# Kernel tuning notes

Hardware: AMD Instinct MI355X
Metric: run time of the kernel (lower is better)

Reference implementation:

```python
import jax, jax.numpy as jnp
import numpy as np

N, R, H, OUT = 512, 16, 16, 1
EPSILON = 1e-6
CUTOFF = 5.0  # ExpNormalSmearing cutoff_upper (cutoff_lower = 0)


def exp_normal_smearing(dist):
    # dist: (N, N, 1) -> (N, N, R); TorchMD-Net style ExpNormalSmearing
    start = jnp.exp(-CUTOFF)
    means = jnp.linspace(start, 1.0, R, dtype=dist.dtype)
    beta = (2.0 / R * (1.0 - start)) ** -2
    cutoff = 0.5 * (jnp.cos(dist * jnp.pi / CUTOFF) + 1.0) * (dist < CUTOFF)
    return cutoff * jnp.exp(-beta * (jnp.exp(-dist) - means) ** 2)


def setup_inputs() -> dict:
    key = jax.random.key(0)
    ks = jax.random.split(key, 9)
    s_in = 1.0 / np.sqrt(H * H)
    s_h = 1.0 / np.sqrt(H)
    return {
        "x": jax.random.normal(ks[0], (N, 3), jnp.float32) * 1.5,
        "W": jax.random.normal(ks[1], (2, N, R, H), jnp.float32) * 0.1,
        "W1": jax.random.normal(ks[2], (H, H * H), jnp.float32) * s_in,
        "b1": jax.random.normal(ks[3], (H,), jnp.float32) * 0.01,
        "W2": jax.random.normal(ks[4], (4 * R * H, H), jnp.float32) * s_h,
        "W3": jax.random.normal(ks[5], (H, H * H), jnp.float32) * s_in,
        "b3": jax.random.normal(ks[6], (H,), jnp.float32) * 0.01,
        "W4": jax.random.normal(ks[7], (OUT, H), jnp.float32) * s_h,
        "b4": jax.random.normal(ks[8], (OUT,), jnp.float32) * 0.01,
    }


def reference(x, W, W1, b1, W2, W3, b3, W4, b4):
    K, Q = W[0], W[1]                               # (N, R, H) each
    diff = x[:, None, :] - x[None, :, :]            # (N, N, 3)
    nsq = jnp.sum(diff * diff, axis=-1, keepdims=True) + EPSILON
    norm = jnp.sqrt(nsq)                            # (N, N, 1)
    diff = diff / nsq                               # note: divided by squared norm (faithful)
    sm = exp_normal_smearing(norm)                  # (N, N, R)
    basis = sm[..., None] * diff[..., None, :]      # (N, N, R, 3)

    bk = jnp.einsum('ijrb,jrc->icb', basis, K)      # (N, H, 3)
    bq = jnp.einsum('ijrb,jrc->icb', basis, Q)
    att = jnp.einsum('ihb,igb->ihg', bk, bq).reshape(N, H * H)
    att = jax.nn.silu(att @ W1.T + b1) @ W2.T       # (N, 4*R*H), second Linear bias-free

    left, right = att[:, : 2 * R * H], att[:, 2 * R * H:]
    pair = left[:, None, :] + right[None, :, :]     # (N, N, 2*R*H)
    K2 = pair[..., : R * H].reshape(N, N, R, H)
    Q2 = pair[..., R * H:].reshape(N, N, R, H)

    bk = jnp.einsum('ijrb,ijrc->icb', basis, K2)    # (N, H, 3)
    bq = jnp.einsum('ijrb,ijrc->icb', basis, Q2)
    att = jnp.einsum('ihb,igb->ihg', bk, bq).reshape(N, H * H)
    return jax.nn.silu(att @ W3.T + b3) @ W4.T + b4  # (N, OUT)
```

## Files before the change

kernel.cpp:

```cpp
#include <hip/hip_runtime.h>
#include <hip/hip_bf16.h>
#include <math.h>

#define NN 512

#define START 0.006737946999085467f
#define STEP  ((1.0f - START) * (1.0f/15.0f))
#define SB    (0.125f * (1.0f - START))
#define BETA  (1.0f/(SB*SB))
#define LOG2E 1.4426950408889634f
#define NB    (-(BETA)*LOG2E)


__global__ __launch_bounds__(256) void k1a(const float* __restrict__ x,
                                           const float* __restrict__ W,
                                           float* __restrict__ part1)
{
    const int ib = blockIdx.x & 127, jsH = blockIdx.x >> 7;
    const int i0 = ib * 4;
    const int tid = threadIdx.x;
    const int c = tid & 15, js = tid >> 4;
    const int lane = tid & 63, wv = tid >> 6;

    __shared__ float lG[1328];
    __shared__ float lP[256];
    __shared__ float s_part[4][16][26];

    const int gi = tid >> 6, gj = (tid >> 2) & 15, grq = tid & 3;
    const float gxi0 = x[(i0+gi)*3+0];
    const float gxi1 = x[(i0+gi)*3+1];
    const float gxi2 = x[(i0+gi)*3+2];

    float acc[24];
    #pragma unroll
    for (int v = 0; v < 24; ++v) acc[v] = 0.f;

    for (int jt = 0; jt < 4; ++jt) {
        const int jb = jsH*64 + jt*16;
        __syncthreads();

        {
            float d0 = gxi0 - x[(jb+gj)*3+0];
            float d1 = gxi1 - x[(jb+gj)*3+1];
            float d2 = gxi2 - x[(jb+gj)*3+2];
            float nsq = fmaf(d0,d0, fmaf(d1,d1, fmaf(d2,d2, 1e-6f)));
            float rs  = __builtin_amdgcn_rsqf(nsq);
            float nrm = nsq * rs;
            float inv = rs * rs;
            float cutv = 0.f;
            if (nrm < 5.0f) cutv = 0.5f*(__cosf(nrm*0.6283185307179586f)+1.0f);
            float en = exp2f(-LOG2E * nrm);
            if (grq == 0) {
                float4 dP; dP.x = d0*inv; dP.y = d1*inv; dP.z = d2*inv; dP.w = 0.f;
                *reinterpret_cast<float4*>(&lP[(gi*16+gj)*4]) = dP;
            }
            float4 g4;
            {
                float t0 = en - (START + STEP*(float)(grq*4+0));
                float t1 = en - (START + STEP*(float)(grq*4+1));
                float t2 = en - (START + STEP*(float)(grq*4+2));
                float t3 = en - (START + STEP*(float)(grq*4+3));
                g4.x = cutv * exp2f(NB*t0*t0);
                g4.y = cutv * exp2f(NB*t1*t1);
                g4.z = cutv * exp2f(NB*t2*t2);
                g4.w = cutv * exp2f(NB*t3*t3);
            }
            *reinterpret_cast<float4*>(&lG[gi*328 + gj*20 + grq*4]) = g4;
        }
        __syncthreads();

        const float* Kr = W + (size_t)(jb+js)*256 + c;
        const float* Qr = Kr + NN*256;
        float kk[16], qq[16];
        #pragma unroll
        for (int r = 0; r < 16; ++r) { kk[r] = Kr[r*16]; qq[r] = Qr[r*16]; }

        #pragma unroll
        for (int i = 0; i < 4; ++i) {
            const float4* gp = reinterpret_cast<const float4*>(&lG[i*328 + js*20]);
            float4 gA = gp[0], gB = gp[1], gC = gp[2], gD = gp[3];
            float tk = 0.f, tq = 0.f;
            tk = fmaf(gA.x,kk[ 0], tk); tq = fmaf(gA.x,qq[ 0], tq);
            tk = fmaf(gA.y,kk[ 1], tk); tq = fmaf(gA.y,qq[ 1], tq);
            tk = fmaf(gA.z,kk[ 2], tk); tq = fmaf(gA.z,qq[ 2], tq);
            tk = fmaf(gA.w,kk[ 3], tk); tq = fmaf(gA.w,qq[ 3], tq);
            tk = fmaf(gB.x,kk[ 4], tk); tq = fmaf(gB.x,qq[ 4], tq);
            tk = fmaf(gB.y,kk[ 5], tk); tq = fmaf(gB.y,qq[ 5], tq);
            tk = fmaf(gB.z,kk[ 6], tk); tq = fmaf(gB.z,qq[ 6], tq);
            tk = fmaf(gB.w,kk[ 7], tk); tq = fmaf(gB.w,qq[ 7], tq);
            tk = fmaf(gC.x,kk[ 8], tk); tq = fmaf(gC.x,qq[ 8], tq);
            tk = fmaf(gC.y,kk[ 9], tk); tq = fmaf(gC.y,qq[ 9], tq);
            tk = fmaf(gC.z,kk[10], tk); tq = fmaf(gC.z,qq[10], tq);
            tk = fmaf(gC.w,kk[11], tk); tq = fmaf(gC.w,qq[11], tq);
            tk = fmaf(gD.x,kk[12], tk); tq = fmaf(gD.x,qq[12], tq);
            tk = fmaf(gD.y,kk[13], tk); tq = fmaf(gD.y,qq[13], tq);
            tk = fmaf(gD.z,kk[14], tk); tq = fmaf(gD.z,qq[14], tq);
            tk = fmaf(gD.w,kk[15], tk); tq = fmaf(gD.w,qq[15], tq);
            float4 dd = *reinterpret_cast<const float4*>(&lP[(i*16+js)*4]);
            acc[i*6+0] = fmaf(tk, dd.x, acc[i*6+0]);
            acc[i*6+1] = fmaf(tk, dd.y, acc[i*6+1]);
            acc[i*6+2] = fmaf(tk, dd.z, acc[i*6+2]);
            acc[i*6+3] = fmaf(tq, dd.x, acc[i*6+3]);
            acc[i*6+4] = fmaf(tq, dd.y, acc[i*6+4]);
            acc[i*6+5] = fmaf(tq, dd.z, acc[i*6+5]);
        }
    }

    #pragma unroll
    for (int v = 0; v < 24; ++v) {
        float t = acc[v];
        t += __shfl_xor(t, 16);
        t += __shfl_xor(t, 32);
        if (lane < 16) s_part[wv][c][v] = t;
    }
    __syncthreads();

    for (int v = tid; v < 384; v += 256) {
        int i = v / 96, o = v - i*96;
        int kq = o / 48, rem = o - kq*48;
        int b = rem >> 4, c2 = rem & 15;
        int f = i*6 + kq*3 + b;
        float sum = s_part[0][c2][f] + s_part[1][c2][f]
                  + s_part[2][c2][f] + s_part[3][c2][f];
        part1[(i0+i)*768 + jsH*96 + o] = sum;
    }
}

__global__ __launch_bounds__(256) void k1b(const float* __restrict__ part1,
                                           const float* __restrict__ W1,
                                           const float* __restrict__ b1,
                                           const float* __restrict__ W2,
                                           float* __restrict__ att2)
{
    const int i = blockIdx.x;
    const int tid = threadIdx.x;
    __shared__ float s_bkq[96];
    __shared__ float s_att[256];
    __shared__ float s_z[16][16];
    __shared__ float s_a1[16];

    if (tid < 96) {
        const float* p = part1 + i*768 + tid;
        float s = 0.f;
        #pragma unroll
        for (int k = 0; k < 8; ++k) s += p[k*96];
        s_bkq[tid] = s;
    }
    __syncthreads();

    {
        int h = tid >> 4, g = tid & 15;
        s_att[tid] = s_bkq[     h]*s_bkq[48+     g]
                   + s_bkq[16 + h]*s_bkq[48+16 + g]
                   + s_bkq[32 + h]*s_bkq[48+32 + g];
    }
    __syncthreads();

    {
        int h = tid & 15, seg = tid >> 4;
        const float* w1 = W1 + h*256 + seg*16;
        const float* a  = s_att + seg*16;
        float p = 0.f;
        #pragma unroll
        for (int k = 0; k < 16; ++k) p = fmaf(a[k], w1[k], p);
        s_z[seg][h] = p;
    }
    __syncthreads();

    if (tid < 16) {
        float z = b1[tid];
        #pragma unroll
        for (int seg = 0; seg < 16; ++seg) z += s_z[seg][tid];
        s_a1[tid] = z / (1.0f + __expf(-z));
    }
    __syncthreads();

    float a1[16];
    #pragma unroll
    for (int cc = 0; cc < 16; ++cc) a1[cc] = s_a1[cc];
    #pragma unroll
    for (int p = 0; p < 4; ++p) {
        int o = tid + p*256;
        const float4* w2 = reinterpret_cast<const float4*>(W2 + o*16);
        float4 wa = w2[0], wb = w2[1], wc = w2[2], wd = w2[3];
        float accv = wa.x*a1[0] + wa.y*a1[1] + wa.z*a1[2] + wa.w*a1[3]
                   + wb.x*a1[4] + wb.y*a1[5] + wb.z*a1[6] + wb.w*a1[7]
                   + wc.x*a1[8] + wc.y*a1[9] + wc.z*a1[10]+ wc.w*a1[11]
                   + wd.x*a1[12]+ wd.y*a1[13]+ wd.z*a1[14]+ wd.w*a1[15];
        att2[i*1024 + o] = accv;
    }
}

__global__ __launch_bounds__(256) void k2a(const float* __restrict__ x,
                                           const float* __restrict__ att2,
                                           float* __restrict__ part2)
{
    const int ib = blockIdx.x & 127, jsH = blockIdx.x >> 7;
    const int i0 = ib * 4;
    const int tid = threadIdx.x;
    const int c = tid & 15, js = tid >> 4;
    const int lane = tid & 63, wv = tid >> 6;

    __shared__ float lG[1328];
    __shared__ float lP[256];
    __shared__ float s_part[4][16][38];

    const int gi = tid >> 6, gj = (tid >> 2) & 15, grq = tid & 3;
    const float gxi0 = x[(i0+gi)*3+0];
    const float gxi1 = x[(i0+gi)*3+1];
    const float gxi2 = x[(i0+gi)*3+2];

    float acc[36];
    #pragma unroll
    for (int v = 0; v < 36; ++v) acc[v] = 0.f;

    for (int jt = 0; jt < 4; ++jt) {
        const int jb = jsH*64 + jt*16;
        __syncthreads();

        {
            float d0 = gxi0 - x[(jb+gj)*3+0];
            float d1 = gxi1 - x[(jb+gj)*3+1];
            float d2 = gxi2 - x[(jb+gj)*3+2];
            float nsq = fmaf(d0,d0, fmaf(d1,d1, fmaf(d2,d2, 1e-6f)));
            float rs  = __builtin_amdgcn_rsqf(nsq);
            float nrm = nsq * rs;
            float inv = rs * rs;
            float cutv = 0.f;
            if (nrm < 5.0f) cutv = 0.5f*(__cosf(nrm*0.6283185307179586f)+1.0f);
            float en = exp2f(-LOG2E * nrm);
            if (grq == 0) {
                float4 dP; dP.x = d0*inv; dP.y = d1*inv; dP.z = d2*inv; dP.w = 0.f;
                *reinterpret_cast<float4*>(&lP[(gi*16+gj)*4]) = dP;
            }
            float4 g4;
            {
                float t0 = en - (START + STEP*(float)(grq*4+0));
                float t1 = en - (START + STEP*(float)(grq*4+1));
                float t2 = en - (START + STEP*(float)(grq*4+2));
                float t3 = en - (START + STEP*(float)(grq*4+3));
                g4.x = cutv * exp2f(NB*t0*t0);
                g4.y = cutv * exp2f(NB*t1*t1);
                g4.z = cutv * exp2f(NB*t2*t2);
                g4.w = cutv * exp2f(NB*t3*t3);
            }
            *reinterpret_cast<float4*>(&lG[gi*328 + gj*20 + grq*4]) = g4;
        }
        __syncthreads();

        const float* Rk = att2 + (size_t)(jb+js)*1024 + 512 + c;
        const float* Rq = Rk + 256;
        float kk[16], qq[16];
        #pragma unroll
        for (int r = 0; r < 16; ++r) { kk[r] = Rk[r*16]; qq[r] = Rq[r*16]; }

        #pragma unroll
        for (int i = 0; i < 4; ++i) {
            const float4* gp = reinterpret_cast<const float4*>(&lG[i*328 + js*20]);
            float4 gA = gp[0], gB = gp[1], gC = gp[2], gD = gp[3];
            float tk = 0.f, tq = 0.f;
            tk = fmaf(gA.x,kk[ 0], tk); tq = fmaf(gA.x,qq[ 0], tq);
            tk = fmaf(gA.y,kk[ 1], tk); tq = fmaf(gA.y,qq[ 1], tq);
            tk = fmaf(gA.z,kk[ 2], tk); tq = fmaf(gA.z,qq[ 2], tq);
            tk = fmaf(gA.w,kk[ 3], tk); tq = fmaf(gA.w,qq[ 3], tq);
            tk = fmaf(gB.x,kk[ 4], tk); tq = fmaf(gB.x,qq[ 4], tq);
            tk = fmaf(gB.y,kk[ 5], tk); tq = fmaf(gB.y,qq[ 5], tq);
            tk = fmaf(gB.z,kk[ 6], tk); tq = fmaf(gB.z,qq[ 6], tq);
            tk = fmaf(gB.w,kk[ 7], tk); tq = fmaf(gB.w,qq[ 7], tq);
            tk = fmaf(gC.x,kk[ 8], tk); tq = fmaf(gC.x,qq[ 8], tq);
            tk = fmaf(gC.y,kk[ 9], tk); tq = fmaf(gC.y,qq[ 9], tq);
            tk = fmaf(gC.z,kk[10], tk); tq = fmaf(gC.z,qq[10], tq);
            tk = fmaf(gC.w,kk[11], tk); tq = fmaf(gC.w,qq[11], tq);
            tk = fmaf(gD.x,kk[12], tk); tq = fmaf(gD.x,qq[12], tq);
            tk = fmaf(gD.y,kk[13], tk); tq = fmaf(gD.y,qq[13], tq);
            tk = fmaf(gD.z,kk[14], tk); tq = fmaf(gD.z,qq[14], tq);
            tk = fmaf(gD.w,kk[15], tk); tq = fmaf(gD.w,qq[15], tq);
            float4 dd = *reinterpret_cast<const float4*>(&lP[(i*16+js)*4]);
            acc[i*6+0] = fmaf(tk, dd.x, acc[i*6+0]);
            acc[i*6+1] = fmaf(tk, dd.y, acc[i*6+1]);
            acc[i*6+2] = fmaf(tk, dd.z, acc[i*6+2]);
            acc[i*6+3] = fmaf(tq, dd.x, acc[i*6+3]);
            acc[i*6+4] = fmaf(tq, dd.y, acc[i*6+4]);
            acc[i*6+5] = fmaf(tq, dd.z, acc[i*6+5]);
            float gc = lG[i*328 + js*20 + c];
            acc[24+i*3+0] = fmaf(gc, dd.x, acc[24+i*3+0]);
            acc[24+i*3+1] = fmaf(gc, dd.y, acc[24+i*3+1]);
            acc[24+i*3+2] = fmaf(gc, dd.z, acc[24+i*3+2]);
        }
    }

    #pragma unroll
    for (int v = 0; v < 36; ++v) {
        float t = acc[v];
        t += __shfl_xor(t, 16);
        t += __shfl_xor(t, 32);
        if (lane < 16) s_part[wv][c][v] = t;
    }
    __syncthreads();

    for (int v = tid; v < 576; v += 256) {
        int i = v / 144, o = v - i*144;
        int c2, f;
        if (o < 96) {
            int kq = o / 48, rem = o - kq*48;
            int b = rem >> 4; c2 = rem & 15;
            f = i*6 + kq*3 + b;
        } else {
            int oS = o - 96;
            int r = oS / 3, b = oS - r*3;
            c2 = r;
            f = 24 + i*3 + b;
        }
        float sum = s_part[0][c2][f] + s_part[1][c2][f]
                  + s_part[2][c2][f] + s_part[3][c2][f];
        part2[(i0+i)*1152 + jsH*144 + o] = sum;
    }
}

__global__ __launch_bounds__(256) void k2b(const float* __restrict__ att2,
                                           const float* __restrict__ part2,
                                           const float* __restrict__ W3,
                                           const float* __restrict__ b3,
                                           const float* __restrict__ W4,
                                           const float* __restrict__ b4,
                                           float* __restrict__ out)
{
    const int i = blockIdx.x;
    const int tid = threadIdx.x;
    __shared__ float s_red[144];
    __shared__ float s_att[256];
    __shared__ float s_z[16][16];
    __shared__ float s_a1[16];

    if (tid < 144) {
        const float* p = part2 + i*1152 + tid;
        float s = 0.f;
        #pragma unroll
        for (int k = 0; k < 8; ++k) s += p[k*144];
        s_red[tid] = s;
    }
    __syncthreads();

    if (tid < 96) {
        int kq = tid / 48, rem = tid - kq*48;
        int b = rem >> 4, c = rem & 15;
        const float* lrow = att2 + i*1024 + kq*256 + c;
        float add = 0.f;
        #pragma unroll
        for (int r = 0; r < 16; ++r)
            add = fmaf(lrow[r*16], s_red[96 + r*3 + b], add);
        s_red[tid] += add;
    }
    __syncthreads();

    {
        int h = tid >> 4, g = tid & 15;
        s_att[tid] = s_red[     h]*s_red[48+     g]
                   + s_red[16 + h]*s_red[48+16 + g]
                   + s_red[32 + h]*s_red[48+32 + g];
    }
    __syncthreads();

    {
        int h = tid & 15, seg = tid >> 4;
        const float* w3 = W3 + h*256 + seg*16;
        const float* a  = s_att + seg*16;
        float p = 0.f;
        #pragma unroll
        for (int k = 0; k < 16; ++k) p = fmaf(a[k], w3[k], p);
        s_z[seg][h] = p;
    }
    __syncthreads();

    if (tid < 16) {
        float z = b3[tid];
        #pragma unroll
        for (int seg = 0; seg < 16; ++seg) z += s_z[seg][tid];
        s_a1[tid] = z / (1.0f + __expf(-z));
    }
    __syncthreads();

    if (tid == 0) {
        float accv = b4[0];
        #pragma unroll
        for (int cc = 0; cc < 16; ++cc) accv = fmaf(s_a1[cc], W4[cc], accv);
        out[i] = accv;
    }
}

extern "C" void kernel_launch(void* const* d_in, const int* in_sizes, int n_in,
                              void* d_out, int out_size, void* d_ws, size_t ws_size,
                              hipStream_t stream) {
    (void)in_sizes; (void)n_in; (void)out_size; (void)ws_size;
    const float* x  = (const float*)d_in[0];
    const float* W  = (const float*)d_in[1];
    const float* W1 = (const float*)d_in[2];
    const float* b1 = (const float*)d_in[3];
    const float* W2 = (const float*)d_in[4];
    const float* W3 = (const float*)d_in[5];
    const float* b3 = (const float*)d_in[6];
    const float* W4 = (const float*)d_in[7];
    const float* b4 = (const float*)d_in[8];

    float* att2  = (float*)d_ws;
    float* part1 = att2 + 512*1024;
    float* part2 = part1 + 512*768;
    float* out   = (float*)d_out;

    k1a<<<1024, 256, 0, stream>>>(x, W, part1);
    k1b<<<512, 256, 0, stream>>>(part1, W1, b1, W2, att2);
    k2a<<<1024, 256, 0, stream>>>(x, att2, part2);
    k2b<<<512, 256, 0, stream>>>(att2, part2, W3, b3, W4, b4, out);
}
```

Measured before the change: 126.0 us.

## Transpose K/Q weights for vector loads, store smearing in fp16, compute once

```diff
diff --git a/kernel.cpp b/kernel.cpp
--- a/kernel.cpp
+++ b/kernel.cpp
@@ -1,5 +1,6 @@
 #include <hip/hip_runtime.h>
 #include <hip/hip_bf16.h>
+#include <hip/hip_fp16.h>
 #include <math.h>
 
 #define NN 512
@@ -12,91 +13,102 @@
 #define NB    (-(BETA)*LOG2E)
 
 
-__global__ __launch_bounds__(256) void k1a(const float* __restrict__ x,
-                                           const float* __restrict__ W,
-                                           float* __restrict__ part1)
+__global__ __launch_bounds__(256) void k0(const float* __restrict__ W,
+                                          float* __restrict__ Wt)
 {
-    const int ib = blockIdx.x & 127, jsH = blockIdx.x >> 7;
+    __shared__ float ldsb[256];
+    const int row = blockIdx.x;
+    ldsb[threadIdx.x] = W[(size_t)row*256 + threadIdx.x];
+    __syncthreads();
+    const int c = threadIdx.x >> 4, r = threadIdx.x & 15;
+    Wt[(size_t)row*256 + threadIdx.x] = ldsb[r*16 + c];
+}
+
+__global__ __launch_bounds__(256,3) void k1a(const float* __restrict__ x,
+                                             const float* __restrict__ Wt,
+                                             float* __restrict__ part1)
+{
+    const int ib = blockIdx.x & 127, jc = blockIdx.x >> 7;
     const int i0 = ib * 4;
     const int tid = threadIdx.x;
     const int c = tid & 15, js = tid >> 4;
     const int lane = tid & 63, wv = tid >> 6;
 
-    __shared__ float lG[1328];
-    __shared__ float lP[256];
+    __shared__ __half lG[4][64][16];
+    __shared__ float4 lP[4][64];
     __shared__ float s_part[4][16][26];
 
-    const int gi = tid >> 6, gj = (tid >> 2) & 15, grq = tid & 3;
-    const float gxi0 = x[(i0+gi)*3+0];
-    const float gxi1 = x[(i0+gi)*3+1];
-    const float gxi2 = x[(i0+gi)*3+2];
+    {
+        const int pi = tid >> 6, pj = tid & 63;
+        const int jg = jc*64 + pj;
+        const float xi0 = x[(i0+pi)*3+0], xi1 = x[(i0+pi)*3+1], xi2 = x[(i0+pi)*3+2];
+        float d0 = xi0 - x[jg*3+0];
+        float d1 = xi1 - x[jg*3+1];
+        float d2 = xi2 - x[jg*3+2];
+        float nsq = fmaf(d0,d0, fmaf(d1,d1, fmaf(d2,d2, 1e-6f)));
+        float rs  = __builtin_amdgcn_rsqf(nsq);
+        float nrm = nsq * rs;
+        float inv = rs * rs;
+        float cutv = 0.f;
+        if (nrm < 5.0f) cutv = 0.5f*(__cosf(nrm*0.6283185307179586f)+1.0f);
+        float en = exp2f(-LOG2E * nrm);
+        lP[pi][pj] = make_float4(d0*inv, d1*inv, d2*inv, 0.f);
+        __half2* dst = reinterpret_cast<__half2*>(&lG[pi][pj][0]);
+        #pragma unroll
+        for (int r2 = 0; r2 < 8; ++r2) {
+            float t0 = en - (START + STEP*(float)(2*r2+0));
+            float t1 = en - (START + STEP*(float)(2*r2+1));
+            dst[r2] = __floats2half2_rn(cutv*exp2f(NB*t0*t0),
+                                        cutv*exp2f(NB*t1*t1));
+        }
+    }
+    __syncthreads();
 
     float acc[24];
     #pragma unroll
     for (int v = 0; v < 24; ++v) acc[v] = 0.f;
 
-    for (int jt = 0; jt < 4; ++jt) {
-        const int jb = jsH*64 + jt*16;
-        __syncthreads();
-
-        {
-            float d0 = gxi0 - x[(jb+gj)*3+0];
-            float d1 = gxi1 - x[(jb+gj)*3+1];
-            float d2 = gxi2 - x[(jb+gj)*3+2];
-            float nsq = fmaf(d0,d0, fmaf(d1,d1, fmaf(d2,d2, 1e-6f)));
-            float rs  = __builtin_amdgcn_rsqf(nsq);
-            float nrm = nsq * rs;
-            float inv = rs * rs;
-            float cutv = 0.f;
-            if (nrm < 5.0f) cutv = 0.5f*(__cosf(nrm*0.6283185307179586f)+1.0f);
-            float en = exp2f(-LOG2E * nrm);
-            if (grq == 0) {
-                float4 dP; dP.x = d0*inv; dP.y = d1*inv; dP.z = d2*inv; dP.w = 0.f;
-                *reinterpret_cast<float4*>(&lP[(gi*16+gj)*4]) = dP;
-            }
-            float4 g4;
-            {
-                float t0 = en - (START + STEP*(float)(grq*4+0));
-                float t1 = en - (START + STEP*(float)(grq*4+1));
-                float t2 = en - (START + STEP*(float)(grq*4+2));
-                float t3 = en - (START + STEP*(float)(grq*4+3));
-                g4.x = cutv * exp2f(NB*t0*t0);
-                g4.y = cutv * exp2f(NB*t1*t1);
-                g4.z = cutv * exp2f(NB*t2*t2);
-                g4.w = cutv * exp2f(NB*t3*t3);
-            }
-            *reinterpret_cast<float4*>(&lG[gi*328 + gj*20 + grq*4]) = g4;
-        }
-        __syncthreads();
-
-        const float* Kr = W + (size_t)(jb+js)*256 + c;
-        const float* Qr = Kr + NN*256;
-        float kk[16], qq[16];
-        #pragma unroll
-        for (int r = 0; r < 16; ++r) { kk[r] = Kr[r*16]; qq[r] = Qr[r*16]; }
+    #pragma unroll
+    for (int t = 0; t < 4; ++t) {
+        const int jl = js + 16*t;
+        const int jg = jc*64 + jl;
+        const float4* Kp = reinterpret_cast<const float4*>(Wt + (size_t)jg*256 + c*16);
+        const float4* Qp = reinterpret_cast<const float4*>(Wt + (size_t)NN*256 + (size_t)jg*256 + c*16);
+        float4 ka = Kp[0], kb = Kp[1], kc = Kp[2], kd = Kp[3];
+        float4 qa = Qp[0], qb = Qp[1], qc = Qp[2], qd = Qp[3];
 
         #pragma unroll
         for (int i = 0; i < 4; ++i) {
-            const float4* gp = reinterpret_cast<const float4*>(&lG[i*328 + js*20]);
-            float4 gA = gp[0], gB = gp[1], gC = gp[2], gD = gp[3];
-            float tk = 0.f, tq = 0.f;
-            tk = fmaf(gA.x,kk[ 0], tk); tq = fmaf(gA.x,qq[ 0], tq);
-            tk = fmaf(gA.y,kk[ 1], tk); tq = fmaf(gA.y,qq[ 1], tq);
-            tk = fmaf(gA.z,kk[ 2], tk); tq = fmaf(gA.z,qq[ 2], tq);
-            tk = fmaf(gA.w,kk[ 3], tk); tq = fmaf(gA.w,qq[ 3], tq);
-            tk = fmaf(gB.x,kk[ 4], tk); tq = fmaf(gB.x,qq[ 4], tq);
-            tk = fmaf(gB.y,kk[ 5], tk); tq = fmaf(gB.y,qq[ 5], tq);
-            tk = fmaf(gB.z,kk[ 6], tk); tq = fmaf(gB.z,qq[ 6], tq);
-            tk = fmaf(gB.w,kk[ 7], tk); tq = fmaf(gB.w,qq[ 7], tq);
-            tk = fmaf(gC.x,kk[ 8], tk); tq = fmaf(gC.x,qq[ 8], tq);
-            tk = fmaf(gC.y,kk[ 9], tk); tq = fmaf(gC.y,qq[ 9], tq);
-            tk = fmaf(gC.z,kk[10], tk); tq = fmaf(gC.z,qq[10], tq);
-            tk = fmaf(gC.w,kk[11], tk); tq = fmaf(gC.w,qq[11], tq);
-            tk = fmaf(gD.x,kk[12], tk); tq = fmaf(gD.x,qq[12], tq);
-            tk = fmaf(gD.y,kk[13], tk); tq = fmaf(gD.y,qq[13], tq);
-            tk = fmaf(gD.z,kk[14], tk); tq = fmaf(gD.z,qq[14], tq);
-            tk = fmaf(gD.w,kk[15], tk); tq = fmaf(gD.w,qq[15], tq);
-            float4 dd = *reinterpret_cast<const float4*>(&lP[(i*16+js)*4]);
+            const float4* gp = reinterpret_cast<const float4*>(&lG[i][jl][0]);
+            float4 g0 = gp[0], g1 = gp[1];
+            const __half2* h0 = reinterpret_cast<const __half2*>(&g0);
+            const __half2* h1 = reinterpret_cast<const __half2*>(&g1);
+            float2 p0 = __half22float2(h0[0]);
+            float2 p1 = __half22float2(h0[1]);
+            float2 p2 = __half22float2(h0[2]);
+            float2 p3 = __half22float2(h0[3]);
+            float2 p4 = __half22float2(h1[0]);
+            float2 p5 = __half22float2(h1[1]);
+            float2 p6 = __half22float2(h1[2]);
+            float2 p7 = __half22float2(h1[3]);
+            float tk, tq;
+            tk = p0.x*ka.x; tq = p0.x*qa.x;
+            tk = fmaf(p0.y,ka.y,tk); tq = fmaf(p0.y,qa.y,tq);
+            tk = fmaf(p1.x,ka.z,tk); tq = fmaf(p1.x,qa.z,tq);
+            tk = fmaf(p1.y,ka.w,tk); tq = fmaf(p1.y,qa.w,tq);
+            tk = fmaf(p2.x,kb.x,tk); tq = fmaf(p2.x,qb.x,tq);
+            tk = fmaf(p2.y,kb.y,tk); tq = fmaf(p2.y,qb.y,tq);
+            tk = fmaf(p3.x,kb.z,tk); tq = fmaf(p3.x,qb.z,tq);
+            tk = fmaf(p3.y,kb.w,tk); tq = fmaf(p3.y,qb.w,tq);
+            tk = fmaf(p4.x,kc.x,tk); tq = fmaf(p4.x,qc.x,tq);
+            tk = fmaf(p4.y,kc.y,tk); tq = fmaf(p4.y,qc.y,tq);
+            tk = fmaf(p5.x,kc.z,tk); tq = fmaf(p5.x,qc.z,tq);
+            tk = fmaf(p5.y,kc.w,tk); tq = fmaf(p5.y,qc.w,tq);
+            tk = fmaf(p6.x,kd.x,tk); tq = fmaf(p6.x,qd.x,tq);
+            tk = fmaf(p6.y,kd.y,tk); tq = fmaf(p6.y,qd.y,tq);
+            tk = fmaf(p7.x,kd.z,tk); tq = fmaf(p7.x,qd.z,tq);
+            tk = fmaf(p7.y,kd.w,tk); tq = fmaf(p7.y,qd.w,tq);
+            float4 dd = lP[i][jl];
             acc[i*6+0] = fmaf(tk, dd.x, acc[i*6+0]);
             acc[i*6+1] = fmaf(tk, dd.y, acc[i*6+1]);
             acc[i*6+2] = fmaf(tk, dd.z, acc[i*6+2]);
@@ -122,7 +134,7 @@
         int f = i*6 + kq*3 + b;
         float sum = s_part[0][c2][f] + s_part[1][c2][f]
                   + s_part[2][c2][f] + s_part[3][c2][f];
-        part1[(i0+i)*768 + jsH*96 + o] = sum;
+        part1[(i0+i)*768 + jc*96 + o] = sum;
     }
 }
 
@@ -130,7 +142,7 @@
                                            const float* __restrict__ W1,
                                            const float* __restrict__ b1,
                                            const float* __restrict__ W2,
-                                           float* __restrict__ att2)
+                                           float* __restrict__ att2t)
 {
     const int i = blockIdx.x;
     const int tid = threadIdx.x;
@@ -187,102 +199,104 @@
                    + wb.x*a1[4] + wb.y*a1[5] + wb.z*a1[6] + wb.w*a1[7]
                    + wc.x*a1[8] + wc.y*a1[9] + wc.z*a1[10]+ wc.w*a1[11]
                    + wd.x*a1[12]+ wd.y*a1[13]+ wd.z*a1[14]+ wd.w*a1[15];
-        att2[i*1024 + o] = accv;
-    }
-}
-
-__global__ __launch_bounds__(256) void k2a(const float* __restrict__ x,
-                                           const float* __restrict__ att2,
-                                           float* __restrict__ part2)
+        att2t[i*1024 + ((o>>8)*256) + ((o&15)*16) + ((o>>4)&15)] = accv;
+    }
+}
+
+__global__ __launch_bounds__(256,3) void k2a(const float* __restrict__ x,
+                                             const float* __restrict__ att2t,
+                                             float* __restrict__ part2)
 {
-    const int ib = blockIdx.x & 127, jsH = blockIdx.x >> 7;
+    const int ib = blockIdx.x & 127, jc = blockIdx.x >> 7;
     const int i0 = ib * 4;
     const int tid = threadIdx.x;
     const int c = tid & 15, js = tid >> 4;
     const int lane = tid & 63, wv = tid >> 6;
 
-    __shared__ float lG[1328];
-    __shared__ float lP[256];
+    __shared__ __half lG[4][64][16];
+    __shared__ float4 lP[4][64];
     __shared__ float s_part[4][16][38];
 
-    const int gi = tid >> 6, gj = (tid >> 2) & 15, grq = tid & 3;
-    const float gxi0 = x[(i0+gi)*3+0];
-    const float gxi1 = x[(i0+gi)*3+1];
-    const float gxi2 = x[(i0+gi)*3+2];
+    {
+        const int pi = tid >> 6, pj = tid & 63;
+        const int jg = jc*64 + pj;
+        const float xi0 = x[(i0+pi)*3+0], xi1 = x[(i0+pi)*3+1], xi2 = x[(i0+pi)*3+2];
+        float d0 = xi0 - x[jg*3+0];
+        float d1 = xi1 - x[jg*3+1];
+        float d2 = xi2 - x[jg*3+2];
+        float nsq = fmaf(d0,d0, fmaf(d1,d1, fmaf(d2,d2, 1e-6f)));
+        float rs  = __builtin_amdgcn_rsqf(nsq);
+        float nrm = nsq * rs;
+        float inv = rs * rs;
+        float cutv = 0.f;
+        if (nrm < 5.0f) cutv = 0.5f*(__cosf(nrm*0.6283185307179586f)+1.0f);
+        float en = exp2f(-LOG2E * nrm);
+        lP[pi][pj] = make_float4(d0*inv, d1*inv, d2*inv, 0.f);
+        __half2* dst = reinterpret_cast<__half2*>(&lG[pi][pj][0]);
+        #pragma unroll
+        for (int r2 = 0; r2 < 8; ++r2) {
+            float t0 = en - (START + STEP*(float)(2*r2+0));
+            float t1 = en - (START + STEP*(float)(2*r2+1));
+            dst[r2] = __floats2half2_rn(cutv*exp2f(NB*t0*t0),
+                                        cutv*exp2f(NB*t1*t1));
+        }
+    }
+    __syncthreads();
 
     float acc[36];
     #pragma unroll
     for (int v = 0; v < 36; ++v) acc[v] = 0.f;
 
-    for (int jt = 0; jt < 4; ++jt) {
-        const int jb = jsH*64 + jt*16;
-        __syncthreads();
-
-        {
-            float d0 = gxi0 - x[(jb+gj)*3+0];
-            float d1 = gxi1 - x[(jb+gj)*3+1];
-            float d2 = gxi2 - x[(jb+gj)*3+2];
-            float nsq = fmaf(d0,d0, fmaf(d1,d1, fmaf(d2,d2, 1e-6f)));
-            float rs  = __builtin_amdgcn_rsqf(nsq);
-            float nrm = nsq * rs;
-            float inv = rs * rs;
-            float cutv = 0.f;
-            if (nrm < 5.0f) cutv = 0.5f*(__cosf(nrm*0.6283185307179586f)+1.0f);
-            float en = exp2f(-LOG2E * nrm);
-            if (grq == 0) {
-                float4 dP; dP.x = d0*inv; dP.y = d1*inv; dP.z = d2*inv; dP.w = 0.f;
-                *reinterpret_cast<float4*>(&lP[(gi*16+gj)*4]) = dP;
-            }
-            float4 g4;
-            {
-                float t0 = en - (START + STEP*(float)(grq*4+0));
-                float t1 = en - (START + STEP*(float)(grq*4+1));
-                float t2 = en - (START + STEP*(float)(grq*4+2));
-                float t3 = en - (START + STEP*(float)(grq*4+3));
-                g4.x = cutv * exp2f(NB*t0*t0);
-                g4.y = cutv * exp2f(NB*t1*t1);
-                g4.z = cutv * exp2f(NB*t2*t2);
-                g4.w = cutv * exp2f(NB*t3*t3);
-            }
-            *reinterpret_cast<float4*>(&lG[gi*328 + gj*20 + grq*4]) = g4;
-        }
-        __syncthreads();
-
-        const float* Rk = att2 + (size_t)(jb+js)*1024 + 512 + c;
-        const float* Rq = Rk + 256;
-        float kk[16], qq[16];
-        #pragma unroll
-        for (int r = 0; r < 16; ++r) { kk[r] = Rk[r*16]; qq[r] = Rq[r*16]; }
+    #pragma unroll
+    for (int t = 0; t < 4; ++t) {
+        const int jl = js + 16*t;
+        const int jg = jc*64 + jl;
+        const float4* Kp = reinterpret_cast<const float4*>(att2t + (size_t)jg*1024 + 512 + c*16);
+        const float4* Qp = reinterpret_cast<const float4*>(att2t + (size_t)jg*1024 + 768 + c*16);
+        float4 ka = Kp[0], kb = Kp[1], kc = Kp[2], kd = Kp[3];
+        float4 qa = Qp[0], qb = Qp[1], qc = Qp[2], qd = Qp[3];
 
         #pragma unroll
         for (int i = 0; i < 4; ++i) {
-            const float4* gp = reinterpret_cast<const float4*>(&lG[i*328 + js*20]);
-            float4 gA = gp[0], gB = gp[1], gC = gp[2], gD = gp[3];
-            float tk = 0.f, tq = 0.f;
-            tk = fmaf(gA.x,kk[ 0], tk); tq = fmaf(gA.x,qq[ 0], tq);
-            tk = fmaf(gA.y,kk[ 1], tk); tq = fmaf(gA.y,qq[ 1], tq);
-            tk = fmaf(gA.z,kk[ 2], tk); tq = fmaf(gA.z,qq[ 2], tq);
-            tk = fmaf(gA.w,kk[ 3], tk); tq = fmaf(gA.w,qq[ 3], tq);
-            tk = fmaf(gB.x,kk[ 4], tk); tq = fmaf(gB.x,qq[ 4], tq);
-            tk = fmaf(gB.y,kk[ 5], tk); tq = fmaf(gB.y,qq[ 5], tq);
-            tk = fmaf(gB.z,kk[ 6], tk); tq = fmaf(gB.z,qq[ 6], tq);
-            tk = fmaf(gB.w,kk[ 7], tk); tq = fmaf(gB.w,qq[ 7], tq);
-            tk = fmaf(gC.x,kk[ 8], tk); tq = fmaf(gC.x,qq[ 8], tq);
-            tk = fmaf(gC.y,kk[ 9], tk); tq = fmaf(gC.y,qq[ 9], tq);
-            tk = fmaf(gC.z,kk[10], tk); tq = fmaf(gC.z,qq[10], tq);
-            tk = fmaf(gC.w,kk[11], tk); tq = fmaf(gC.w,qq[11], tq);
-            tk = fmaf(gD.x,kk[12], tk); tq = fmaf(gD.x,qq[12], tq);
-            tk = fmaf(gD.y,kk[13], tk); tq = fmaf(gD.y,qq[13], tq);
-            tk = fmaf(gD.z,kk[14], tk); tq = fmaf(gD.z,qq[14], tq);
-            tk = fmaf(gD.w,kk[15], tk); tq = fmaf(gD.w,qq[15], tq);
-            float4 dd = *reinterpret_cast<const float4*>(&lP[(i*16+js)*4]);
+            const float4* gp = reinterpret_cast<const float4*>(&lG[i][jl][0]);
+            float4 g0 = gp[0], g1 = gp[1];
+            const __half2* h0 = reinterpret_cast<const __half2*>(&g0);
+            const __half2* h1 = reinterpret_cast<const __half2*>(&g1);
+            float2 p0 = __half22float2(h0[0]);
+            float2 p1 = __half22float2(h0[1]);
+            float2 p2 = __half22float2(h0[2]);
+            float2 p3 = __half22float2(h0[3]);
+            float2 p4 = __half22float2(h1[0]);
+            float2 p5 = __half22float2(h1[1]);
+            float2 p6 = __half22float2(h1[2]);
+            float2 p7 = __half22float2(h1[3]);
+            float tk, tq;
+            tk = p0.x*ka.x; tq = p0.x*qa.x;
+            tk = fmaf(p0.y,ka.y,tk); tq = fmaf(p0.y,qa.y,tq);
+            tk = fmaf(p1.x,ka.z,tk); tq = fmaf(p1.x,qa.z,tq);
+            tk = fmaf(p1.y,ka.w,tk); tq = fmaf(p1.y,qa.w,tq);
+            tk = fmaf(p2.x,kb.x,tk); tq = fmaf(p2.x,qb.x,tq);
+            tk = fmaf(p2.y,kb.y,tk); tq = fmaf(p2.y,qb.y,tq);
+            tk = fmaf(p3.x,kb.z,tk); tq = fmaf(p3.x,qb.z,tq);
+            tk = fmaf(p3.y,kb.w,tk); tq = fmaf(p3.y,qb.w,tq);
+            tk = fmaf(p4.x,kc.x,tk); tq = fmaf(p4.x,qc.x,tq);
+            tk = fmaf(p4.y,kc.y,tk); tq = fmaf(p4.y,qc.y,tq);
+            tk = fmaf(p5.x,kc.z,tk); tq = fmaf(p5.x,qc.z,tq);
+            tk = fmaf(p5.y,kc.w,tk); tq = fmaf(p5.y,qc.w,tq);
+            tk = fmaf(p6.x,kd.x,tk); tq = fmaf(p6.x,qd.x,tq);
+            tk = fmaf(p6.y,kd.y,tk); tq = fmaf(p6.y,qd.y,tq);
+            tk = fmaf(p7.x,kd.z,tk); tq = fmaf(p7.x,qd.z,tq);
+            tk = fmaf(p7.y,kd.w,tk); tq = fmaf(p7.y,qd.w,tq);
+            float4 dd = lP[i][jl];
             acc[i*6+0] = fmaf(tk, dd.x, acc[i*6+0]);
             acc[i*6+1] = fmaf(tk, dd.y, acc[i*6+1]);
             acc[i*6+2] = fmaf(tk, dd.z, acc[i*6+2]);
             acc[i*6+3] = fmaf(tq, dd.x, acc[i*6+3]);
             acc[i*6+4] = fmaf(tq, dd.y, acc[i*6+4]);
             acc[i*6+5] = fmaf(tq, dd.z, acc[i*6+5]);
-            float gc = lG[i*328 + js*20 + c];
+            __half2 hcv = *reinterpret_cast<const __half2*>(&lG[i][jl][c & 14]);
+            float2 fc = __half22float2(hcv);
+            float gc = (c & 1) ? fc.y : fc.x;
             acc[24+i*3+0] = fmaf(gc, dd.x, acc[24+i*3+0]);
             acc[24+i*3+1] = fmaf(gc, dd.y, acc[24+i*3+1]);
             acc[24+i*3+2] = fmaf(gc, dd.z, acc[24+i*3+2]);
@@ -313,11 +327,11 @@
         }
         float sum = s_part[0][c2][f] + s_part[1][c2][f]
                   + s_part[2][c2][f] + s_part[3][c2][f];
-        part2[(i0+i)*1152 + jsH*144 + o] = sum;
-    }
-}
-
-__global__ __launch_bounds__(256) void k2b(const float* __restrict__ att2,
+        part2[(i0+i)*1152 + jc*144 + o] = sum;
+    }
+}
+
+__global__ __launch_bounds__(256) void k2b(const float* __restrict__ att2t,
                                            const float* __restrict__ part2,
                                            const float* __restrict__ W3,
                                            const float* __restrict__ b3,
@@ -343,12 +357,26 @@
 
     if (tid < 96) {
         int kq = tid / 48, rem = tid - kq*48;
-        int b = rem >> 4, c = rem & 15;
-        const float* lrow = att2 + i*1024 + kq*256 + c;
+        int b = rem >> 4, cc = rem & 15;
+        const float4* lrow = reinterpret_cast<const float4*>(att2t + i*1024 + kq*256 + cc*16);
+        float4 A = lrow[0], B = lrow[1], C = lrow[2], D = lrow[3];
         float add = 0.f;
-        #pragma unroll
-        for (int r = 0; r < 16; ++r)
-            add = fmaf(lrow[r*16], s_red[96 + r*3 + b], add);
+        add = fmaf(A.x, s_red[96+ 0*3+b], add);
+        add = fmaf(A.y, s_red[96+ 1*3+b], add);
+        add = fmaf(A.z, s_red[96+ 2*3+b], add);
+        add = fmaf(A.w, s_red[96+ 3*3+b], add);
+        add = fmaf(B.x, s_red[96+ 4*3+b], add);
+        add = fmaf(B.y, s_red[96+ 5*3+b], add);
+        add = fmaf(B.z, s_red[96+ 6*3+b], add);
+        add = fmaf(B.w, s_red[96+ 7*3+b], add);
+        add = fmaf(C.x, s_red[96+ 8*3+b], add);
+        add = fmaf(C.y, s_red[96+ 9*3+b], add);
+        add = fmaf(C.z, s_red[96+10*3+b], add);
+        add = fmaf(C.w, s_red[96+11*3+b], add);
+        add = fmaf(D.x, s_red[96+12*3+b], add);
+        add = fmaf(D.y, s_red[96+13*3+b], add);
+        add = fmaf(D.z, s_red[96+14*3+b], add);
+        add = fmaf(D.w, s_red[96+15*3+b], add);
         s_red[tid] += add;
     }
     __syncthreads();
@@ -402,13 +430,15 @@
     const float* W4 = (const float*)d_in[7];
     const float* b4 = (const float*)d_in[8];
 
-    float* att2  = (float*)d_ws;
-    float* part1 = att2 + 512*1024;
+    float* att2t = (float*)d_ws;
+    float* part1 = att2t + 512*1024;
     float* part2 = part1 + 512*768;
+    float* Wt    = part2 + 512*1152;
     float* out   = (float*)d_out;
 
-    k1a<<<1024, 256, 0, stream>>>(x, W, part1);
-    k1b<<<512, 256, 0, stream>>>(part1, W1, b1, W2, att2);
-    k2a<<<1024, 256, 0, stream>>>(x, att2, part2);
-    k2b<<<512, 256, 0, stream>>>(att2, part2, W3, b3, W4, b4, out);
-}
+    k0 <<<1024, 256, 0, stream>>>(W, Wt);
+    k1a<<<1024, 256, 0, stream>>>(x, Wt, part1);
+    k1b<<< 512, 256, 0, stream>>>(part1, W1, b1, W2, att2t);
+    k2a<<<1024, 256, 0, stream>>>(x, att2t, part2);
+    k2b<<< 512, 256, 0, stream>>>(att2t, part2, W3, b3, W4, b4, out);
+}
```

New measurement: 384.0 us. 3.05x slower.
